# Performance work log

Hardware: AMD Instinct MI355X
Metric: run time of the kernel (lower is better)

## Reference

```python
import jax, jax.numpy as jnp
import numpy as np

L0, L1, L2 = 32, 16, 8
NS, NB = 512, 256
CUT = 7.0
N, E, G = 16384, 131072, 16
FEAT = L0 + 3 * L1 + 5 * L2  # 120


def setup_inputs() -> dict:
    key = jax.random.key(0)
    ks = jax.random.split(key, 16)
    rn = lambda k, s, sc=1.0: jax.random.normal(k, s, jnp.float32) * sc
    inp = {}
    inp['nodes'] = rn(ks[0], (N, FEAT))
    inp['pos'] = rn(ks[1], (N, 3)) * 5.0
    inp['cell'] = rn(ks[2], (G, 3, 3))
    inp['edge_shift'] = rn(ks[3], (E, 3))
    # tensor-product path weights (e3nn FullyConnectedTensorProduct, uvw mode)
    inp['W0'] = rn(ks[4], (L0, L0, NS))
    inp['W1'] = rn(ks[5], (L1, L1, NS))
    inp['W2'] = rn(ks[6], (L2, L2, NS))
    inp['ln_g'] = jnp.ones((NS,), jnp.float32)
    inp['ln_b'] = jnp.zeros((NS,), jnp.float32)
    inp['df_w1'] = rn(ks[7], (NB, 1024), NB ** -0.5)
    inp['df_b1'] = jnp.zeros((1024,), jnp.float32)
    inp['df_w2'] = rn(ks[8], (1024, NS), 1024 ** -0.5)
    inp['df_b2'] = jnp.zeros((NS,), jnp.float32)
    inp['mi_w1'] = rn(ks[9], (NS, 1024), NS ** -0.5)
    inp['mi_b1'] = jnp.zeros((1024,), jnp.float32)
    inp['mi_w2'] = rn(ks[10], (1024, 1024), 1024 ** -0.5)
    inp['mi_b2'] = jnp.zeros((1024,), jnp.float32)
    inp['mo_w'] = rn(ks[11], (1024, 1), 1024 ** -0.5)
    inp['mo_b'] = jnp.zeros((1,), jnp.float32)
    inp['edge_index'] = jax.random.randint(ks[12], (2, E), 0, N)
    inp['batch_vec'] = jnp.sort(jax.random.randint(ks[13], (N,), 0, G))
    return inp


def _split_irreps(x):
    x0 = x[:, :L0]                                   # (E, L0) scalars 0e
    x1 = x[:, L0:L0 + 3 * L1].reshape(-1, L1, 3)      # (E, L1, 3) vectors 1o
    x2 = x[:, L0 + 3 * L1:].reshape(-1, L2, 5)        # (E, L2, 5) 2e
    return x0, x1, x2


def reference(nodes, pos, cell, edge_shift, W0, W1, W2, ln_g, ln_b,
              df_w1, df_b1, df_w2, df_b2, mi_w1, mi_b1, mi_w2, mi_b2,
              mo_w, mo_b, edge_index, batch_vec):
    src, dst = edge_index[0], edge_index[1]
    # periodic-image translation vector per edge
    bcell = cell[batch_vec[src]]                      # (E,3,3)
    tvec = jnp.einsum('ei,eij->ej', edge_shift, bcell)
    radvec = pos[dst] - pos[src] + tvec               # (E,3)
    dist = jnp.linalg.norm(radvec, axis=1, keepdims=True)  # (E,1)
    r = 1.0 / (dist + 1e-6)
    # Bessel radial embedding with cutoff CUT, NB basis functions
    n = jnp.arange(1, NB + 1, dtype=jnp.float32)
    emb = jnp.sqrt(2.0 / CUT) * jnp.sin(n * jnp.pi * r / CUT) / r  # (E,NB)
    distfilter = jax.nn.silu(emb @ df_w1 + df_b1) @ df_w2 + df_b2  # (E,NS)

    # symmetrized fully-connected tensor product -> 0e scalars
    # 0.5*(tp(xs,xd)+tp(xd,xs)) == contraction of euv with symmetrized W
    xs0, xs1, xs2 = _split_irreps(nodes[src])
    xd0, xd1, xd2 = _split_irreps(nodes[dst])
    fan = jnp.sqrt(jnp.float32(L0 * L0 + L1 * L1 + L2 * L2))  # element path norm
    sym = lambda W: 0.5 * (W + W.transpose(1, 0, 2))
    e0 = jnp.einsum('eu,ev->euv', xs0, xd0)
    mixed = jnp.einsum('euv,uvw->ew', e0, sym(W0)) / fan
    e1 = jnp.einsum('eui,evi->euv', xs1, xd1)
    mixed = mixed + jnp.einsum('euv,uvw->ew', e1, sym(W1)) / (fan * jnp.sqrt(3.0))
    e2 = jnp.einsum('eui,evi->euv', xs2, xd2)
    mixed = mixed + jnp.einsum('euv,uvw->ew', e2, sym(W2)) / (fan * jnp.sqrt(5.0))

    # LayerNorm over numscalars
    mu = jnp.mean(mixed, axis=-1, keepdims=True)
    var = jnp.mean((mixed - mu) ** 2, axis=-1, keepdims=True)
    mixednorm = (mixed - mu) * jax.lax.rsqrt(var + 1e-5) * ln_g + ln_b

    reg = mixednorm * distfilter
    h = jax.nn.silu(reg @ mi_w1 + mi_b1)
    h = jax.nn.silu(h @ mi_w2 + mi_b2)
    return h @ mo_w + mo_b  # (E,1)
```

## Files before the change

### kernel.cpp

```cpp
#include <hip/hip_runtime.h>

#define EE 131072
#define NNODE 16384
#define FEAT 120
#define NS 512
#define NB 256
#define KCAT 1344

typedef unsigned short u16;
typedef __bf16 bf16x8 __attribute__((ext_vector_type(8)));
typedef float f32x4 __attribute__((ext_vector_type(4)));
typedef unsigned short ushort8 __attribute__((ext_vector_type(8)));
typedef unsigned short us4 __attribute__((ext_vector_type(4)));

__device__ __forceinline__ float b2f(u16 u) {
  union { unsigned int i; float f; } x; x.i = ((unsigned int)u) << 16; return x.f;
}
__device__ __forceinline__ u16 f2b(float f) {
  union { float f; unsigned int i; } x; x.f = f;
  unsigned int lsb = (x.i >> 16) & 1u;
  x.i += 0x7fffu + lsb;
  return (u16)(x.i >> 16);
}
__device__ __forceinline__ u16 f2b_fast(float f) {
  __bf16 h = (__bf16)f;
  union { __bf16 h; u16 u; } x; x.h = h; return x.u;
}
__device__ __forceinline__ float rdany(const void* p, long i, int f32) {
  return f32 ? ((const float*)p)[i] : b2f(((const u16*)p)[i]);
}

__device__ __forceinline__ void gload16(const u16* g, u16* l) {
  __builtin_amdgcn_global_load_lds(
      (__attribute__((address_space(1))) void*)(u16*)g,
      (__attribute__((address_space(3))) void*)l, 16, 0, 0);
}

struct PrepArgs {
  long cum[20];
  const void* src[19];
  u16* dst[19];
  float* outf;
  int* flag;
  const u16* nodes;
};

__global__ __launch_bounds__(256) void megaprep(PrepArgs a) {
  __shared__ int scnt[4];
  {
    u16 v = a.nodes[threadIdx.x];
    int e = (v >> 7) & 0xFF;
    unsigned long long b = __ballot(e >= 0x48);
    if ((threadIdx.x & 63) == 0) scnt[threadIdx.x >> 6] = __popcll(b);
  }
  __syncthreads();
  const int f32 = (scnt[0] + scnt[1] + scnt[2] + scnt[3]) >= 16;
  if (blockIdx.x == 0 && threadIdx.x == 0) *a.flag = f32;

  long i = (long)blockIdx.x * 256 + threadIdx.x;
  const long total = a.cum[19];
  if (i < total) {
    int s = 0;
    while (i >= a.cum[s + 1]) s++;
    long local = i - a.cum[s];
    a.dst[s][local] = f32 ? f2b(((const float*)a.src[s])[local])
                          : ((const u16*)a.src[s])[local];
  } else {
    long j = i - total;
    if (j < EE) a.outf[j] = 0.f;
  }
}

struct WprepArgs {
  const u16* tin[4];
  u16* tout[4];
  const u16 *W0, *W1, *W2;
  u16* wcT;
};

__device__ __forceinline__ void do_transpose(const u16* in, u16* out, int R, int C, int rem) {
  __shared__ u16 tile[32][33];
  const int bx = C >> 5;
  const int c0 = (rem % bx) * 32, r0 = (rem / bx) * 32;
  const int tx = threadIdx.x & 31, ty = threadIdx.x >> 5;
  for (int i = 0; i < 32; i += 8) {
    int r = r0 + ty + i, c = c0 + tx;
    if (r < R && c < C) tile[ty + i][tx] = in[(long)r * C + c];
  }
  __syncthreads();
  for (int i = 0; i < 32; i += 8) {
    int r = r0 + tx, c = c0 + ty + i;
    if (r < R && c < C) out[(long)c * R + r] = tile[tx][ty + i];
  }
}

__global__ __launch_bounds__(256) void wprep(WprepArgs a) {
  int b = blockIdx.x;
  if (b < 256) { do_transpose(a.tin[0], a.tout[0], 256, 1024, b); return; }
  b -= 256;
  if (b < 512) { do_transpose(a.tin[1], a.tout[1], 1024, 512, b); return; }
  b -= 512;
  if (b < 512) { do_transpose(a.tin[2], a.tout[2], 512, 1024, b); return; }
  b -= 512;
  if (b < 1024) { do_transpose(a.tin[3], a.tout[3], 1024, 1024, b); return; }
  b -= 1024;
  int idx = b * 256 + threadIdx.x;
  if (idx >= NS * KCAT) return;
  int w = idx / KCAT, k = idx - w * KCAT;
  const float fan = 36.66060556f;
  float val;
  if (k < 1024) {
    int u = k >> 5, v = k & 31;
    val = 0.5f * (b2f(a.W0[(u * 32 + v) * NS + w]) + b2f(a.W0[(v * 32 + u) * NS + w])) / fan;
  } else if (k < 1280) {
    int j = k - 1024;
    int u = j >> 4, v = j & 15;
    val = 0.5f * (b2f(a.W1[(u * 16 + v) * NS + w]) + b2f(a.W1[(v * 16 + u) * NS + w])) /
          (fan * 1.7320508076f);
  } else {
    int j = k - 1280;
    int u = j >> 3, v = j & 7;
    val = 0.5f * (b2f(a.W2[(u * 8 + v) * NS + w]) + b2f(a.W2[(v * 8 + u) * NS + w])) /
          (fan * 2.2360679775f);
  }
  a.wcT[idx] = f2b(val);
}

__global__ __launch_bounds__(256) void edge_prep(
    const u16* __restrict__ nodes, const void* __restrict__ pos, const void* __restrict__ cell,
    const void* __restrict__ shift, const int* __restrict__ eidx, const int* __restrict__ batch,
    u16* __restrict__ emb, u16* __restrict__ ocat, int e0, const int* __restrict__ flag) {
  const int wave = threadIdx.x >> 6, lane = threadIdx.x & 63;
  const int el = blockIdx.x * 4 + wave;
  const int e = e0 + el;
  const int f32 = *flag;
  __shared__ u16 sxs[4][FEAT], sxd[4][FEAT];
  const int src = eidx[e], dst = eidx[EE + e];
  for (int i = lane; i < FEAT; i += 64) {
    sxs[wave][i] = nodes[(long)src * FEAT + i];
    sxd[wave][i] = nodes[(long)dst * FEAT + i];
  }
  __syncthreads();
  const int b = batch[src];
  float s0 = rdany(shift, (long)e * 3, f32), s1 = rdany(shift, (long)e * 3 + 1, f32),
        s2 = rdany(shift, (long)e * 3 + 2, f32);
  float d2 = 0.f;
#pragma unroll
  for (int j = 0; j < 3; j++) {
    float tv = s0 * rdany(cell, b * 9 + j, f32) + s1 * rdany(cell, b * 9 + 3 + j, f32) +
               s2 * rdany(cell, b * 9 + 6 + j, f32);
    float rv = rdany(pos, dst * 3 + j, f32) - rdany(pos, src * 3 + j, f32) + tv;
    d2 += rv * rv;
  }
  float dist = sqrtf(d2);
  float r = 1.0f / (dist + 1e-6f);
  const float c0 = 0.5345224838f;
  const float pi7 = 0.44879895051f;
  {
    us4 ev;
#pragma unroll
    for (int j = 0; j < 4; j++) {
      int n = lane * 4 + j;
      ev[j] = f2b(c0 * sinf((float)(n + 1) * pi7 * r) / r);
    }
    *(us4*)&emb[(long)el * NB + lane * 4] = ev;
  }
  const u16* xs = sxs[wave];
  const u16* xd = sxd[wave];
  u16* orow = ocat + (long)el * KCAT;
  {
    const float xu = b2f(xs[lane >> 1]);
    const int v0 = (lane & 1) * 16;
    const ushort8 xd0 = *(const ushort8*)&xd[v0];
    const ushort8 xd1 = *(const ushort8*)&xd[v0 + 8];
    ushort8 o0, o1;
#pragma unroll
    for (int j = 0; j < 8; j++) {
      o0[j] = f2b(xu * b2f(xd0[j]));
      o1[j] = f2b(xu * b2f(xd1[j]));
    }
    *(ushort8*)&orow[lane * 16] = o0;
    *(ushort8*)&orow[lane * 16 + 8] = o1;
  }
  {
    const int u = lane >> 2;
    us4 o;
#pragma unroll
    for (int j = 0; j < 4; j++) {
      const int v = (lane & 3) * 4 + j;
      float s = 0.f;
#pragma unroll
      for (int i = 0; i < 3; i++) s += b2f(xs[32 + u * 3 + i]) * b2f(xd[32 + v * 3 + i]);
      o[j] = f2b(s);
    }
    *(us4*)&orow[1024 + lane * 4] = o;
  }
  {
    int u = lane >> 3, v = lane & 7;
    float s = 0.f;
#pragma unroll
    for (int i = 0; i < 5; i++) s += b2f(xs[80 + u * 5 + i]) * b2f(xd[80 + v * 5 + i]);
    orow[1280 + lane] = f2b(s);
  }
}

#define STGA(buf, kk)                                                      \
  do {                                                                     \
    _Pragma("unroll") for (int i = 0; i < 4; i++)                          \
        gload16(Ag + (i * 32) * (long)K + (kk), &lA[buf][i * 2048 + tid * 8]); \
  } while (0)
#define STGB(buf, kk)                                                      \
  do {                                                                     \
    _Pragma("unroll") for (int i = 0; i < 4; i++)                          \
        gload16(Bg + (i * 32) * (long)K + (kk), &lB[buf][i * 2048 + tid * 8]); \
  } while (0)
#define RDA(buf, fm, ks)                                                   \
  (*(const bf16x8*)((const char*)&lA[buf][0] +                             \
                    ((wm * 64 + (fm)*16 + row_l) * 128 + ((ks) ? ir1 : ir0))))
#define RDB(buf, fn, ks)                                                   \
  (*(const bf16x8*)((const char*)&lB[buf][0] +                             \
                    ((wn * 64 + (fn)*16 + row_l) * 128 + ((ks) ? ir1 : ir0))))
#define MF16(a, b, c) __builtin_amdgcn_mfma_f32_16x16x32_bf16(a, b, c, 0, 0, 0)

template <int ACT, int OF32, int HEAD>
__global__ __launch_bounds__(256, 2) void gemm_bt(const u16* __restrict__ A,
                                                  const u16* __restrict__ BT,
                                                  const u16* __restrict__ bias,
                                                  void* __restrict__ Cv,
                                                  const u16* __restrict__ hw,
                                                  float* __restrict__ outf, int N, int K) {
  __shared__ __align__(16) u16 lA[2][8192];
  __shared__ __align__(16) u16 lB[2][8192];
  const int tid = threadIdx.x;
  const int lane = tid & 63;
  const int wave = tid >> 6;
  const int wm = wave >> 1, wn = wave & 1;
  const int row_l = lane & 15;
  const int kq16 = (lane >> 4) << 4;
  const int swz = (row_l & 7) << 4;
  const int ir0 = kq16 ^ swz;
  const int ir1 = (64 + kq16) ^ swz;

  const int nbn = N >> 7;
  int idx = blockIdx.x;
  if ((gridDim.x & 7) == 0) {
    int per = gridDim.x >> 3;
    idx = (blockIdx.x & 7) * per + (blockIdx.x >> 3);
  }
  const int mi = idx / nbn;
  const int ni = idx - mi * nbn;
  const long m0 = (long)mi * 128;
  const int n0 = ni << 7;
  const int nk = K >> 6;

  const int srow = tid >> 3;
  const int gseg = (tid & 7) ^ (srow & 7);
  const u16* Ag = A + (m0 + srow) * (long)K + gseg * 8;
  const u16* Bg = BT + (long)(n0 + srow) * K + gseg * 8;

  f32x4 acc[4][4];
#pragma unroll
  for (int i = 0; i < 4; i++)
#pragma unroll
    for (int j = 0; j < 4; j++)
#pragma unroll
      for (int q = 0; q < 4; q++) acc[i][j][q] = 0.f;

  STGA(0, 0);
  STGB(0, 0);
  asm volatile("s_waitcnt vmcnt(0)" ::: "memory");
  __builtin_amdgcn_s_barrier();

  bf16x8 af[4][2], bf[4][2];

  for (int t = 0; t < nk; ++t) {
    const int cur = t & 1, nxt = cur ^ 1;
    if (t + 1 < nk) {
      STGA(nxt, (t + 1) * 64);
      STGB(nxt, (t + 1) * 64);
    }
#pragma unroll
    for (int f = 0; f < 4; f++) { af[f][0] = RDA(cur, f, 0); af[f][1] = RDA(cur, f, 1); }
#pragma unroll
    for (int g = 0; g < 4; g++) { bf[g][0] = RDB(cur, g, 0); bf[g][1] = RDB(cur, g, 1); }
#pragma unroll
    for (int f = 0; f < 4; f++)
#pragma unroll
      for (int g = 0; g < 4; g++)
#pragma unroll
        for (int ks = 0; ks < 2; ks++)
          acc[f][g] = MF16(af[f][ks], bf[g][ks], acc[f][g]);
    __syncthreads();
  }

  const int rql = (lane >> 4) * 2;
  const int cl = lane & 15;
  float* Cf = (float*)Cv;
  u16* Cb = (u16*)Cv;
  if (HEAD) {
    float bv[4], hv[4];
#pragma unroll
    for (int g = 0; g < 4; g++) {
      const int col = n0 + wn * 64 + g * 16 + cl;
      bv[g] = b2f(bias[col]);
      hv[g] = b2f(hw[col]);
    }
#pragma unroll
    for (int fm = 0; fm < 4; fm++) {
#pragma unroll
      for (int q = 0; q < 4; q++) {
        float s = 0.f;
#pragma unroll
        for (int g = 0; g < 4; g++) {
          float v = acc[fm][g][q] + bv[g];
          if (ACT) v = __fdividef(v, 1.0f + __expf(-v));
          s += v * hv[g];
        }
        s += __shfl_xor(s, 1);
        s += __shfl_xor(s, 2);
        s += __shfl_xor(s, 4);
        s += __shfl_xor(s, 8);
        if (cl == 0) {
          long row = m0 + wm * 64 + fm * 16 + rql * 2 + q;
          atomicAdd(&outf[row], s);
        }
      }
    }
  } else {
#pragma unroll
    for (int fm = 0; fm < 4; fm++) {
#pragma unroll
      for (int g = 0; g < 4; g++) {
        const int col = n0 + wn * 64 + g * 16 + cl;
        const float bvv = bias ? b2f(bias[col]) : 0.0f;
#pragma unroll
        for (int q = 0; q < 4; q++) {
          long row = m0 + wm * 64 + fm * 16 + rql * 2 + q;
          float v = acc[fm][g][q] + bvv;
          if (ACT) v = __fdividef(v, 1.0f + __expf(-v));
          if (OF32)
            Cf[row * N + col] = v;
          else
            Cb[row * N + col] = f2b_fast(v);
        }
      }
    }
  }
}

__global__ __launch_bounds__(256) void ln_mul_k(const float* __restrict__ mixed,
                                                const u16* __restrict__ g,
                                                const u16* __restrict__ bvec,
                                                u16* __restrict__ dfreg) {
  const int wave = threadIdx.x >> 6, lane = threadIdx.x & 63;
  const long e = (long)blockIdx.x * 4 + wave;
  const float* row = mixed + e * NS;
  float x[8];
  f32x4 v0 = *(const f32x4*)&row[lane * 8];
  f32x4 v1 = *(const f32x4*)&row[lane * 8 + 4];
#pragma unroll
  for (int j = 0; j < 4; j++) { x[j] = v0[j]; x[4 + j] = v1[j]; }
  float s = 0.f, sq = 0.f;
#pragma unroll
  for (int j = 0; j < 8; j++) { s += x[j]; sq += x[j] * x[j]; }
  for (int o = 32; o; o >>= 1) { s += __shfl_xor(s, o); sq += __shfl_xor(sq, o); }
  float mu = s * (1.0f / 512.0f);
  float var = sq * (1.0f / 512.0f) - mu * mu;
  float rstd = rsqrtf(var + 1e-5f);
  u16* drow = dfreg + e * NS;
  ushort8 dv = *(const ushort8*)&drow[lane * 8];
  ushort8 ov;
#pragma unroll
  for (int j = 0; j < 8; j++) {
    int c = lane * 8 + j;
    float val = (x[j] - mu) * rstd * b2f(g[c]) + b2f(bvec[c]);
    ov[j] = f2b(val * b2f(dv[j]));
  }
  *(ushort8*)&drow[lane * 8] = ov;
}

__global__ __launch_bounds__(256) void head_finish(const float* __restrict__ outf,
                                                   const u16* __restrict__ b,
                                                   void* __restrict__ out,
                                                   const int* __restrict__ flag) {
  int e = blockIdx.x * 256 + threadIdx.x;
  float v = outf[e] + b2f(b[0]);
  if (*flag)
    ((float*)out)[e] = v;
  else
    ((u16*)out)[e] = f2b(v);
}

extern "C" void kernel_launch(void* const* d_in, const int* in_sizes, int n_in, void* d_out,
                              int out_size, void* d_ws, size_t ws_size, hipStream_t stream) {
  const int* eidx = (const int*)d_in[19];
  const int* batch = (const int*)d_in[20];

  char* ws = (char*)d_ws;
  size_t off = 0;
  auto alloc = [&](size_t bytes) {
    char* p = ws + off;
    off += (bytes + 255) & ~(size_t)255;
    return p;
  };

  int* flag = (int*)alloc(256);
  float* outf = (float*)alloc((size_t)EE * 4);

  PrepArgs pa;
  u16* cv[19];
  long cum = 0;
  for (int i = 0; i < 19; i++) {
    long n = in_sizes[i];
    cv[i] = (u16*)alloc((size_t)n * 2);
    pa.cum[i] = cum;
    pa.src[i] = d_in[i];
    pa.dst[i] = cv[i];
    cum += n;
  }
  pa.cum[19] = cum;
  pa.outf = outf;
  pa.flag = flag;
  pa.nodes = (const u16*)d_in[0];
  {
    long tot = cum + EE;
    megaprep<<<(int)((tot + 255) / 256), 256, 0, stream>>>(pa);
  }
  const u16* nodes = cv[0];
  const u16* ln_g = cv[7];
  const u16* ln_b = cv[8];
  const u16* df_b1 = cv[10];
  const u16* df_b2 = cv[12];
  const u16* mi_b1 = cv[14];
  const u16* mi_b2 = cv[16];
  const u16* mo_w = cv[17];
  const u16* mo_b = cv[18];

  u16* w1T = (u16*)alloc(1024 * 256 * 2);
  u16* w2T = (u16*)alloc(512 * 1024 * 2);
  u16* m1T = (u16*)alloc(1024 * 512 * 2);
  u16* m2T = (u16*)alloc((size_t)1024 * 1024 * 2);
  u16* wcT = (u16*)alloc((size_t)NS * KCAT * 2);

  WprepArgs wa;
  wa.tin[0] = cv[9];  wa.tout[0] = w1T;
  wa.tin[1] = cv[11]; wa.tout[1] = w2T;
  wa.tin[2] = cv[13]; wa.tout[2] = m1T;
  wa.tin[3] = cv[15]; wa.tout[3] = m2T;
  wa.W0 = cv[4]; wa.W1 = cv[5]; wa.W2 = cv[6];
  wa.wcT = wcT;
  wprep<<<4992, 256, 0, stream>>>(wa);

  int nchunk = 1;
  while (nchunk < 64) {
    size_t CHs = (size_t)(EE / nchunk);
    size_t need = off + CHs * 6272 + 8192;
    if (need <= ws_size) break;
    nchunk <<= 1;
  }
  const int CH = EE / nchunk;

  u16* ocat = (u16*)alloc((size_t)CH * KCAT * 2);
  u16* emb = (u16*)alloc((size_t)CH * NB * 2);
  u16* h1 = (u16*)alloc((size_t)CH * 1024 * 2);
  u16* dfb = (u16*)alloc((size_t)CH * NS * 2);
  u16* h2 = ocat;
  float* mixed = (float*)h1;

  const int RB = CH / 128;
  for (int c = 0; c < nchunk; c++) {
    const int eb = c * CH;
    edge_prep<<<CH / 4, 256, 0, stream>>>(nodes, d_in[1], d_in[2], d_in[3], eidx, batch, emb,
                                          ocat, eb, flag);

    gemm_bt<1, 0, 0><<<RB * 8, 256, 0, stream>>>(emb, w1T, df_b1, h1, nullptr, nullptr, 1024, 256);
    gemm_bt<0, 0, 0><<<RB * 4, 256, 0, stream>>>(h1, w2T, df_b2, dfb, nullptr, nullptr, 512, 1024);

    gemm_bt<0, 1, 0><<<RB * 4, 256, 0, stream>>>(ocat, wcT, nullptr, mixed, nullptr, nullptr, 512,
                                                 1344);

    ln_mul_k<<<CH / 4, 256, 0, stream>>>(mixed, ln_g, ln_b, dfb);

    gemm_bt<1, 0, 0><<<RB * 8, 256, 0, stream>>>(dfb, m1T, mi_b1, h2, nullptr, nullptr, 1024, 512);
    gemm_bt<1, 0, 1><<<RB * 8, 256, 0, stream>>>(h2, m2T, mi_b2, nullptr, mo_w, outf + eb, 1024,
                                                 1024);
  }
  head_finish<<<EE / 256, 256, 0, stream>>>(outf, mo_b, d_out, flag);
}
```

Measured before the change: 1.496 ms.

## Enlarge GEMM tiles to 256x256 with 8 waves and read B directly from global

The GEMM kernel moves from 128x128 tiles with 4 waves to 256x256 tiles with 8 waves. Each wave now computes 128x64 outputs (8x4 MFMA fragments). The B operand (weights) is no longer staged through LDS; each wave reads its B fragments straight from global memory, relying on cache hits because the weights are small and shared. The larger tile raises arithmetic intensity on A, but direct global B loads sit on the critical path without prefetch, and 128 accumulator VGPRs per thread may cut occupancy.

```diff
diff --git a/kernel.cpp b/kernel.cpp
--- a/kernel.cpp
+++ b/kernel.cpp
@@ -204,44 +204,35 @@
   }
 }
 
-#define STGA(buf, kk)                                                      \
-  do {                                                                     \
-    _Pragma("unroll") for (int i = 0; i < 4; i++)                          \
-        gload16(Ag + (i * 32) * (long)K + (kk), &lA[buf][i * 2048 + tid * 8]); \
-  } while (0)
-#define STGB(buf, kk)                                                      \
-  do {                                                                     \
-    _Pragma("unroll") for (int i = 0; i < 4; i++)                          \
-        gload16(Bg + (i * 32) * (long)K + (kk), &lB[buf][i * 2048 + tid * 8]); \
-  } while (0)
+#define STGA(buf, h, part, kk)                                             \
+  gload16(Ag + ((h)*128 + (part)*64) * (long)K + (kk),                      \
+          &lA[buf][(h)*8192 + (part)*4096 + tid * 8])
 #define RDA(buf, fm, ks)                                                   \
   (*(const bf16x8*)((const char*)&lA[buf][0] +                             \
-                    ((wm * 64 + (fm)*16 + row_l) * 128 + ((ks) ? ir1 : ir0))))
-#define RDB(buf, fn, ks)                                                   \
-  (*(const bf16x8*)((const char*)&lB[buf][0] +                             \
-                    ((wn * 64 + (fn)*16 + row_l) * 128 + ((ks) ? ir1 : ir0))))
+                    ((wm * 128 + (fm)*16 + row_l) * 128 + ((ks) ? ir1 : ir0))))
+#define RDBG(fn, ks, kk)                                                   \
+  (*(const bf16x8*)&Bl[((fn)*16) * (long)K + (kk) + (ks)*32])
 #define MF16(a, b, c) __builtin_amdgcn_mfma_f32_16x16x32_bf16(a, b, c, 0, 0, 0)
 
 template <int ACT, int OF32, int HEAD>
-__global__ __launch_bounds__(256, 2) void gemm_bt(const u16* __restrict__ A,
+__global__ __launch_bounds__(512, 2) void gemm_bt(const u16* __restrict__ A,
                                                   const u16* __restrict__ BT,
                                                   const u16* __restrict__ bias,
                                                   void* __restrict__ Cv,
                                                   const u16* __restrict__ hw,
                                                   float* __restrict__ outf, int N, int K) {
-  __shared__ __align__(16) u16 lA[2][8192];
-  __shared__ __align__(16) u16 lB[2][8192];
+  __shared__ __align__(16) u16 lA[2][16384];
   const int tid = threadIdx.x;
   const int lane = tid & 63;
   const int wave = tid >> 6;
-  const int wm = wave >> 1, wn = wave & 1;
+  const int wm = wave >> 2, wn = wave & 3;
   const int row_l = lane & 15;
   const int kq16 = (lane >> 4) << 4;
   const int swz = (row_l & 7) << 4;
   const int ir0 = kq16 ^ swz;
   const int ir1 = (64 + kq16) ^ swz;
 
-  const int nbn = N >> 7;
+  const int nbn = N >> 8;
   int idx = blockIdx.x;
   if ((gridDim.x & 7) == 0) {
     int per = gridDim.x >> 3;
@@ -249,42 +240,42 @@
   }
   const int mi = idx / nbn;
   const int ni = idx - mi * nbn;
-  const long m0 = (long)mi * 128;
-  const int n0 = ni << 7;
+  const long m0 = (long)mi * 256;
+  const int n0 = ni << 8;
   const int nk = K >> 6;
 
   const int srow = tid >> 3;
   const int gseg = (tid & 7) ^ (srow & 7);
   const u16* Ag = A + (m0 + srow) * (long)K + gseg * 8;
-  const u16* Bg = BT + (long)(n0 + srow) * K + gseg * 8;
-
-  f32x4 acc[4][4];
-#pragma unroll
-  for (int i = 0; i < 4; i++)
+  const u16* Bl = BT + (long)(n0 + wn * 64 + row_l) * K + ((lane >> 4) << 3);
+
+  f32x4 acc[8][4];
+#pragma unroll
+  for (int i = 0; i < 8; i++)
 #pragma unroll
     for (int j = 0; j < 4; j++)
 #pragma unroll
       for (int q = 0; q < 4; q++) acc[i][j][q] = 0.f;
 
-  STGA(0, 0);
-  STGB(0, 0);
+  STGA(0, 0, 0, 0); STGA(0, 0, 1, 0); STGA(0, 1, 0, 0); STGA(0, 1, 1, 0);
   asm volatile("s_waitcnt vmcnt(0)" ::: "memory");
   __builtin_amdgcn_s_barrier();
 
-  bf16x8 af[4][2], bf[4][2];
+  bf16x8 af[8][2], bf[4][2];
 
   for (int t = 0; t < nk; ++t) {
     const int cur = t & 1, nxt = cur ^ 1;
+    const int kk = t << 6;
     if (t + 1 < nk) {
-      STGA(nxt, (t + 1) * 64);
-      STGB(nxt, (t + 1) * 64);
-    }
-#pragma unroll
-    for (int f = 0; f < 4; f++) { af[f][0] = RDA(cur, f, 0); af[f][1] = RDA(cur, f, 1); }
-#pragma unroll
-    for (int g = 0; g < 4; g++) { bf[g][0] = RDB(cur, g, 0); bf[g][1] = RDB(cur, g, 1); }
-#pragma unroll
-    for (int f = 0; f < 4; f++)
+      STGA(nxt, 0, 0, kk + 64); STGA(nxt, 0, 1, kk + 64);
+      STGA(nxt, 1, 0, kk + 64); STGA(nxt, 1, 1, kk + 64);
+    }
+#pragma unroll
+    for (int g = 0; g < 4; g++) { bf[g][0] = RDBG(g, 0, kk); bf[g][1] = RDBG(g, 1, kk); }
+#pragma unroll
+    for (int f = 0; f < 8; f++) { af[f][0] = RDA(cur, f, 0); af[f][1] = RDA(cur, f, 1); }
+#pragma unroll
+    for (int f = 0; f < 8; f++)
 #pragma unroll
       for (int g = 0; g < 4; g++)
 #pragma unroll
@@ -306,7 +297,7 @@
       hv[g] = b2f(hw[col]);
     }
 #pragma unroll
-    for (int fm = 0; fm < 4; fm++) {
+    for (int fm = 0; fm < 8; fm++) {
 #pragma unroll
       for (int q = 0; q < 4; q++) {
         float s = 0.f;
@@ -321,21 +312,21 @@
         s += __shfl_xor(s, 4);
         s += __shfl_xor(s, 8);
         if (cl == 0) {
-          long row = m0 + wm * 64 + fm * 16 + rql * 2 + q;
+          long row = m0 + wm * 128 + fm * 16 + rql * 2 + q;
           atomicAdd(&outf[row], s);
         }
       }
     }
   } else {
 #pragma unroll
-    for (int fm = 0; fm < 4; fm++) {
+    for (int fm = 0; fm < 8; fm++) {
 #pragma unroll
       for (int g = 0; g < 4; g++) {
         const int col = n0 + wn * 64 + g * 16 + cl;
         const float bvv = bias ? b2f(bias[col]) : 0.0f;
 #pragma unroll
         for (int q = 0; q < 4; q++) {
-          long row = m0 + wm * 64 + fm * 16 + rql * 2 + q;
+          long row = m0 + wm * 128 + fm * 16 + rql * 2 + q;
           float v = acc[fm][g][q] + bvv;
           if (ACT) v = __fdividef(v, 1.0f + __expf(-v));
           if (OF32)
@@ -467,22 +458,22 @@
   u16* h2 = ocat;
   float* mixed = (float*)h1;
 
-  const int RB = CH / 128;
+  const int RB = CH / 256;
   for (int c = 0; c < nchunk; c++) {
     const int eb = c * CH;
     edge_prep<<<CH / 4, 256, 0, stream>>>(nodes, d_in[1], d_in[2], d_in[3], eidx, batch, emb,
                                           ocat, eb, flag);
 
-    gemm_bt<1, 0, 0><<<RB * 8, 256, 0, stream>>>(emb, w1T, df_b1, h1, nullptr, nullptr, 1024, 256);
-    gemm_bt<0, 0, 0><<<RB * 4, 256, 0, stream>>>(h1, w2T, df_b2, dfb, nullptr, nullptr, 512, 1024);
-
-    gemm_bt<0, 1, 0><<<RB * 4, 256, 0, stream>>>(ocat, wcT, nullptr, mixed, nullptr, nullptr, 512,
+    gemm_bt<1, 0, 0><<<RB * 4, 512, 0, stream>>>(emb, w1T, df_b1, h1, nullptr, nullptr, 1024, 256);
+    gemm_bt<0, 0, 0><<<RB * 2, 512, 0, stream>>>(h1, w2T, df_b2, dfb, nullptr, nullptr, 512, 1024);
+
+    gemm_bt<0, 1, 0><<<RB * 2, 512, 0, stream>>>(ocat, wcT, nullptr, mixed, nullptr, nullptr, 512,
                                                  1344);
 
     ln_mul_k<<<CH / 4, 256, 0, stream>>>(mixed, ln_g, ln_b, dfb);
 
-    gemm_bt<1, 0, 0><<<RB * 8, 256, 0, stream>>>(dfb, m1T, mi_b1, h2, nullptr, nullptr, 1024, 512);
-    gemm_bt<1, 0, 1><<<RB * 8, 256, 0, stream>>>(h2, m2T, mi_b2, nullptr, mo_w, outf + eb, 1024,
+    gemm_bt<1, 0, 0><<<RB * 4, 512, 0, stream>>>(dfb, m1T, mi_b1, h2, nullptr, nullptr, 1024, 512);
+    gemm_bt<1, 0, 1><<<RB * 4, 512, 0, stream>>>(h2, m2T, mi_b2, nullptr, mo_w, outf + eb, 1024,
                                                  1024);
   }
   head_finish<<<EE / 256, 256, 0, stream>>>(outf, mo_b, d_out, flag);
```

Result: slower. 1.789 ms (+19.6%).
